# Optimization experiments

Measured on AMD Instinct MI355X. Metric: run time of the kernel, lower is better.

Reference implementation:

```python
import jax, jax.numpy as jnp
import numpy as np

B, L, D, NH = 32, 512, 1024, 1024
T, C = 8, 15          # tables, columns per table
E = T * (1 + C)       # 128 entities (table entity + its column entities)
NCOL = T * C          # 120 column slots == max_entities
K = L // E            # 4 tokens per entity span
TOPK = 6


def setup_inputs() -> dict:
    key = jax.random.key(0)
    ks = jax.random.split(key, 12)
    std = 0.02
    q_enc = jax.random.normal(ks[0], (B, L, D), jnp.float32)
    # contiguous variable-length-style spans: entity e covers tokens [e*K, (e+1)*K)
    entity_tok_idx = jnp.arange(E * K, dtype=jnp.int32).reshape(E, K)
    # entity layout per batch: [tbl0, col0..col14, tbl1, col15..., ...]
    ent = np.arange(E).reshape(T, 1 + C)
    col_entity_idx = jnp.asarray(ent[:, 1:].reshape(-1), jnp.int32)   # [NCOL]
    col_table_idx = jnp.asarray(np.repeat(ent[:, 0], C), jnp.int32)   # [NCOL]
    return {
        "q_enc": q_enc,
        "entity_tok_idx": entity_tok_idx,
        "col_entity_idx": col_entity_idx,
        "col_table_idx": col_table_idx,
        "W_table": jax.random.normal(ks[1], (D, D), jnp.float32) * std,
        "b_table": jnp.zeros((D,), jnp.float32),
        "W_col": jax.random.normal(ks[2], (D, D), jnp.float32) * std,
        "b_col": jnp.zeros((D,), jnp.float32),
        "W_o1": jax.random.normal(ks[3], (D, NH), jnp.float32) * std,
        "b_o1": jnp.zeros((NH,), jnp.float32),
        "W_o2": jax.random.normal(ks[4], (NH, 1), jnp.float32) * std,
        "b_o2": jnp.zeros((1,), jnp.float32),
        "W_t1": jax.random.normal(ks[5], (D, NH), jnp.float32) * std,
        "b_t1": jnp.zeros((NH,), jnp.float32),
        "W_t2": jax.random.normal(ks[6], (NH, TOPK), jnp.float32) * std,
        "b_t2": jnp.zeros((TOPK,), jnp.float32),
    }


def reference(q_enc, entity_tok_idx, col_entity_idx, col_table_idx,
              W_table, b_table, W_col, b_col,
              W_o1, b_o1, W_o2, b_o2,
              W_t1, b_t1, W_t2, b_t2):
    # ragged per-entity token gather + sum pooling (pad+sum in original)
    # q_enc: [B, L, D]; gather -> [B, E, K, D]; segment reduce over K
    encoded_entity = jnp.take(q_enc, entity_tok_idx, axis=1).sum(axis=2)  # [B, E, D]
    # per-column fusion: col_linear(col entity) + table_linear(parent table entity)
    tbl = jnp.einsum("bed,df->bef", encoded_entity[:, col_table_idx], W_table) + b_table
    col = jnp.einsum("bed,df->bef", encoded_entity[:, col_entity_idx], W_col) + b_col
    fused = col + tbl                                                    # [B, NCOL, D]
    att = (jax.nn.relu(fused @ W_o1 + b_o1) @ W_o2 + b_o2)[..., 0]       # [B, NCOL]
    cls = q_enc[:, 0, :]                                                 # [B, D]
    topk = jax.nn.sigmoid(jax.nn.relu(cls @ W_t1 + b_t1) @ W_t2 + b_t2)  # [B, 6]
    return att, topk
```

## Files before the change

kernel.cpp:

```cpp
#include <hip/hip_runtime.h>
#include <hip/hip_bf16.h>

#define BB 32
#define LL 512
#define DD 1024
#define NHD 1024
#define EE 128
#define NCOL 120
#define KTOK 4
#define TOPKN 6
#define MROWS (BB * NCOL)

typedef __attribute__((ext_vector_type(8))) _Float16 f16x8;
typedef __attribute__((ext_vector_type(4))) float f32x4;

__device__ inline ushort f2h(float x) {
    _Float16 h = (_Float16)x;
    union { _Float16 h; ushort u; } c;
    c.h = h;
    return c.u;
}

__global__ __launch_bounds__(256) void ee_kernel(const float* __restrict__ q,
                                                 const int* __restrict__ tok,
                                                 ushort* __restrict__ ee,
                                                 float* __restrict__ att,
                                                 const float* __restrict__ b_o2,
                                                 float* __restrict__ H,
                                                 const float* __restrict__ b_t1) {
    int be = blockIdx.x;
    int b  = be >> 7;
    int e  = be & 127;
    int t  = threadIdx.x;

    if (be < 15) {
        att[be * 256 + t] = b_o2[0];
    } else if (be < 15 + 128) {
        int j = (be - 15) * 256 + t;
        H[j] = b_t1[j & (NHD - 1)];
    }

    const float* qb = q + (size_t)b * LL * DD;
    int t0 = tok[e * KTOK + 0];
    int t1 = tok[e * KTOK + 1];
    int t2 = tok[e * KTOK + 2];
    int t3 = tok[e * KTOK + 3];
    int f = t * 4;
    float4 a = *(const float4*)(qb + (size_t)t0 * DD + f);
    float4 bv = *(const float4*)(qb + (size_t)t1 * DD + f);
    float4 c = *(const float4*)(qb + (size_t)t2 * DD + f);
    float4 d = *(const float4*)(qb + (size_t)t3 * DD + f);
    ushort4 o;
    o.x = f2h(a.x + bv.x + c.x + d.x);
    o.y = f2h(a.y + bv.y + c.y + d.y);
    o.z = f2h(a.z + bv.z + c.z + d.z);
    o.w = f2h(a.w + bv.w + c.w + d.w);
    *(ushort4*)(ee + (size_t)be * DD + f) = o;
}

__global__ __launch_bounds__(256) void pack_w_kernel(
    const float* __restrict__ W0, const float* __restrict__ W1f,
    const float* __restrict__ W2f, ushort* __restrict__ pk0,
    ushort* __restrict__ pk1, ushort* __restrict__ pk2) {
    const float* W = blockIdx.y == 0 ? W0 : (blockIdx.y == 1 ? W1f : W2f);
    ushort* pk     = blockIdx.y == 0 ? pk0 : (blockIdx.y == 1 ? pk1 : pk2);
    int idx = blockIdx.x * 256 + threadIdx.x;
    int l  = idx & 63;
    int kb = (idx >> 6) & 31;
    int nb = idx >> 11;
    int row = kb * 32 + (l >> 4) * 8;
    int col = nb * 16 + (l & 15);
    ushort o[8];
#pragma unroll
    for (int j = 0; j < 8; ++j)
        o[j] = f2h(W[(size_t)(row + j) * NHD + col]);
    ulong2 v;
    v.x = ((ulong)o[0]) | ((ulong)o[1] << 16) | ((ulong)o[2] << 32) | ((ulong)o[3] << 48);
    v.y = ((ulong)o[4]) | ((ulong)o[5] << 16) | ((ulong)o[6] << 32) | ((ulong)o[7] << 48);
    *(ulong2*)(pk + (size_t)idx * 8) = v;
}

__global__ __launch_bounds__(256) void gemm1_kernel(
    const ushort* __restrict__ ee, const int* __restrict__ ci, const int* __restrict__ ti,
    const ushort* __restrict__ Wc_pk, const ushort* __restrict__ Wt_pk,
    const float* __restrict__ bc, const float* __restrict__ bt,
    ushort* __restrict__ fused) {
    int t = threadIdx.x;
    int l = t & 63;
    int w = t >> 6;
    int wm = w >> 1, wn = w & 1;
    int row0 = blockIdx.x * 128 + wm * 64;
    int col0 = blockIdx.y * 64 + wn * 32;
    int nb0  = col0 >> 4;
    int koff = (l >> 4) * 8;

    const ushort* arow0[4];
    const ushort* arow1[4];
#pragma unroll
    for (int m = 0; m < 4; ++m) {
        int r = row0 + m * 16 + (l & 15);
        int b = r / NCOL;
        int i = r - b * NCOL;
        arow0[m] = ee + ((size_t)(b * EE + ci[i])) * DD;
        arow1[m] = ee + ((size_t)(b * EE + ti[i])) * DD;
    }

    f32x4 acc[4][2] = {};

#pragma unroll
    for (int phase = 0; phase < 2; ++phase) {
        const ushort* Wp = phase ? Wt_pk : Wc_pk;
        const ushort* const* ar = phase ? arow1 : arow0;

        f16x8 aA[4], bA[2], aB[4], bB[2];

#define LOAD_FR(AV, BV, kb)                                                     \
        {                                                                       \
            _Pragma("unroll")                                                   \
            for (int m = 0; m < 4; ++m)                                         \
                AV[m] = *(const f16x8*)(ar[m] + (kb) * 32 + koff);              \
            _Pragma("unroll")                                                   \
            for (int n = 0; n < 2; ++n)                                         \
                BV[n] = *(const f16x8*)(Wp + (((size_t)(nb0 + n) * 32 + (kb)) * 64 + l) * 8); \
        }
#define MFMA_FR(AV, BV)                                                         \
        {                                                                       \
            _Pragma("unroll")                                                   \
            for (int m = 0; m < 4; ++m)                                         \
                _Pragma("unroll")                                               \
                for (int n = 0; n < 2; ++n)                                     \
                    acc[m][n] = __builtin_amdgcn_mfma_f32_16x16x32_f16(         \
                        AV[m], BV[n], acc[m][n], 0, 0, 0);                      \
        }

        LOAD_FR(aA, bA, 0)
#pragma unroll 1
        for (int kb = 0; kb < 30; kb += 2) {
            LOAD_FR(aB, bB, kb + 1)
            MFMA_FR(aA, bA)
            LOAD_FR(aA, bA, kb + 2)
            MFMA_FR(aB, bB)
        }
        LOAD_FR(aB, bB, 31)
        MFMA_FR(aA, bA)
        MFMA_FR(aB, bB)
#undef LOAD_FR
#undef MFMA_FR
    }

    float badd[2];
#pragma unroll
    for (int n = 0; n < 2; ++n) {
        int c = col0 + n * 16 + (l & 15);
        badd[n] = bc[c] + bt[c];
    }
    int rlane = (l >> 4) * 4;
#pragma unroll
    for (int m = 0; m < 4; ++m)
#pragma unroll
        for (int n = 0; n < 2; ++n) {
            int c = col0 + n * 16 + (l & 15);
#pragma unroll
            for (int j = 0; j < 4; ++j) {
                int r = row0 + m * 16 + rlane + j;
                fused[(size_t)r * NHD + c] = f2h(acc[m][n][j] + badd[n]);
            }
        }
}

__global__ __launch_bounds__(256) void gemm2_kernel(
    const ushort* __restrict__ fused, const ushort* __restrict__ W1_pk,
    const float* __restrict__ b1, const float* __restrict__ W2,
    float* __restrict__ att) {
    int t = threadIdx.x;
    int l = t & 63;
    int w = t >> 6;
    int wm = w >> 1, wn = w & 1;
    int row0 = blockIdx.x * 128 + wm * 64;
    int col0 = blockIdx.y * 64 + wn * 32;
    int nb0  = col0 >> 4;
    int koff = (l >> 4) * 8;

    const ushort* arow[4];
#pragma unroll
    for (int m = 0; m < 4; ++m)
        arow[m] = fused + (size_t)(row0 + m * 16 + (l & 15)) * NHD;

    f32x4 acc[4][2] = {};
    f16x8 aA[4], bA[2], aB[4], bB[2];

#define LOAD_FR(AV, BV, kb)                                                     \
    {                                                                           \
        _Pragma("unroll")                                                       \
        for (int m = 0; m < 4; ++m)                                             \
            AV[m] = *(const f16x8*)(arow[m] + (kb) * 32 + koff);                \
        _Pragma("unroll")                                                       \
        for (int n = 0; n < 2; ++n)                                             \
            BV[n] = *(const f16x8*)(W1_pk + (((size_t)(nb0 + n) * 32 + (kb)) * 64 + l) * 8); \
    }
#define MFMA_FR(AV, BV)                                                         \
    {                                                                           \
        _Pragma("unroll")                                                       \
        for (int m = 0; m < 4; ++m)                                             \
            _Pragma("unroll")                                                   \
            for (int n = 0; n < 2; ++n)                                         \
                acc[m][n] = __builtin_amdgcn_mfma_f32_16x16x32_f16(             \
                    AV[m], BV[n], acc[m][n], 0, 0, 0);                          \
    }

    LOAD_FR(aA, bA, 0)
#pragma unroll 1
    for (int kb = 0; kb < 30; kb += 2) {
        LOAD_FR(aB, bB, kb + 1)
        MFMA_FR(aA, bA)
        LOAD_FR(aA, bA, kb + 2)
        MFMA_FR(aB, bB)
    }
    LOAD_FR(aB, bB, 31)
    MFMA_FR(aA, bA)
    MFMA_FR(aB, bB)
#undef LOAD_FR
#undef MFMA_FR

    float bo[2], wo[2];
#pragma unroll
    for (int n = 0; n < 2; ++n) {
        int c = col0 + n * 16 + (l & 15);
        bo[n] = b1[c];
        wo[n] = W2[c];
    }
    int rlane = (l >> 4) * 4;
#pragma unroll
    for (int m = 0; m < 4; ++m) {
#pragma unroll
        for (int j = 0; j < 4; ++j) {
            float p = 0.f;
#pragma unroll
            for (int n = 0; n < 2; ++n) {
                float h = fmaxf(acc[m][n][j] + bo[n], 0.f);
                p = fmaf(h, wo[n], p);
            }
            p += __shfl_xor(p, 1);
            p += __shfl_xor(p, 2);
            p += __shfl_xor(p, 4);
            p += __shfl_xor(p, 8);
            if ((l & 15) == 0)
                atomicAdd(&att[row0 + m * 16 + rlane + j], p);
        }
    }
}

__global__ __launch_bounds__(256) void topk_h_kernel(const float* __restrict__ q,
                                                     const float* __restrict__ W1,
                                                     float* __restrict__ H) {
    __shared__ float cls[BB][128];
    __shared__ float wsh[128][17];
    int f0 = blockIdx.x * 16;
    int k0 = blockIdx.y * 128;
    int t = threadIdx.x;
#pragma unroll
    for (int m = 0; m < 16; ++m) {
        int idx = t + m * 256;
        int b = idx >> 7, d = idx & 127;
        cls[b][d] = q[(size_t)b * LL * DD + k0 + d];
    }
#pragma unroll
    for (int m = 0; m < 8; ++m) {
        int idx = t + m * 256;
        int r = idx >> 4, c = idx & 15;
        wsh[r][c] = W1[(size_t)(k0 + r) * NHD + f0 + c];
    }
    __syncthreads();
    int f = t & 15;
    int b0 = t >> 4;
#pragma unroll
    for (int h = 0; h < 2; ++h) {
        int b = b0 + h * 16;
        float s = 0.f;
#pragma unroll 8
        for (int d = 0; d < 128; ++d)
            s = fmaf(cls[b][d], wsh[d][f], s);
        atomicAdd(&H[(size_t)b * NHD + f0 + f], s);
    }
}

__global__ __launch_bounds__(256) void topk_out_kernel(
    const float* __restrict__ H, const float* __restrict__ W2,
    const float* __restrict__ b2, float* __restrict__ outp) {
    __shared__ float red[4][TOPKN];
    int b = blockIdx.x;
    int t = threadIdx.x;
    float part[TOPKN] = {};
#pragma unroll
    for (int m = 0; m < 4; ++m) {
        int f = t + m * 256;
        float h = fmaxf(H[(size_t)b * NHD + f], 0.f);
#pragma unroll
        for (int k = 0; k < TOPKN; ++k)
            part[k] = fmaf(h, W2[f * TOPKN + k], part[k]);
    }
#pragma unroll
    for (int k = 0; k < TOPKN; ++k) {
        float v = part[k];
        for (int off = 1; off < 64; off <<= 1) v += __shfl_xor(v, off);
        part[k] = v;
    }
    int wave = t >> 6, lane = t & 63;
    if (lane == 0)
#pragma unroll
        for (int k = 0; k < TOPKN; ++k) red[wave][k] = part[k];
    __syncthreads();
    if (t == 0)
#pragma unroll
        for (int k = 0; k < TOPKN; ++k) {
            float s = red[0][k] + red[1][k] + red[2][k] + red[3][k] + b2[k];
            outp[b * TOPKN + k] = 1.f / (1.f + __expf(-s));
        }
}

extern "C" void kernel_launch(void* const* d_in, const int* in_sizes, int n_in,
                              void* d_out, int out_size, void* d_ws, size_t ws_size,
                              hipStream_t stream) {
    const float* q_enc   = (const float*)d_in[0];
    const int*   etok    = (const int*)  d_in[1];
    const int*   ci      = (const int*)  d_in[2];
    const int*   ti      = (const int*)  d_in[3];
    const float* W_table = (const float*)d_in[4];
    const float* b_table = (const float*)d_in[5];
    const float* W_col   = (const float*)d_in[6];
    const float* b_col   = (const float*)d_in[7];
    const float* W_o1    = (const float*)d_in[8];
    const float* b_o1    = (const float*)d_in[9];
    const float* W_o2    = (const float*)d_in[10];
    const float* b_o2    = (const float*)d_in[11];
    const float* W_t1    = (const float*)d_in[12];
    const float* b_t1    = (const float*)d_in[13];
    const float* W_t2    = (const float*)d_in[14];
    const float* b_t2    = (const float*)d_in[15];

    float* outp = (float*)d_out;
    float* att  = outp;
    float* topk = outp + MROWS;

    char* ws = (char*)d_ws;
    ushort* ee_h    = (ushort*)(ws);
    ushort* fused   = (ushort*)(ws + 8388608);
    ushort* Wc_pk   = (ushort*)(ws + 16252928);
    ushort* Wt_pk   = (ushort*)(ws + 18350080);
    ushort* Wo1_pk  = (ushort*)(ws + 20447232);
    float*  H       = (float*) (ws + 22544384);

    hipLaunchKernelGGL(ee_kernel, dim3(BB * EE), dim3(256), 0, stream,
                       q_enc, etok, ee_h, att, b_o2, H, b_t1);
    hipLaunchKernelGGL(pack_w_kernel, dim3(512, 3), dim3(256), 0, stream,
                       W_col, W_table, W_o1, Wc_pk, Wt_pk, Wo1_pk);
    hipLaunchKernelGGL(gemm1_kernel, dim3(MROWS / 128, NHD / 64), dim3(256), 0, stream,
                       ee_h, ci, ti, Wc_pk, Wt_pk, b_col, b_table, fused);
    hipLaunchKernelGGL(gemm2_kernel, dim3(MROWS / 128, NHD / 64), dim3(256), 0, stream,
                       fused, Wo1_pk, b_o1, W_o2, att);
    hipLaunchKernelGGL(topk_h_kernel, dim3(64, 8), dim3(256), 0, stream, q_enc, W_t1, H);
    hipLaunchKernelGGL(topk_out_kernel, dim3(BB), dim3(256), 0, stream, H, W_t2, b_t2, topk);
}
```

Baseline: 225.5 us.

## Halve GEMM row tile and deepen register prefetch to three stages

Both GEMM kernels now give each wave a 32x32 output tile instead of 64x32, which doubles the grid to 60x16 blocks. The register pipeline changes from double-buffered to triple-buffered fragment loads, with explicit scalar accumulators. The aim is more blocks and waves across the CUs, plus deeper latency hiding for the direct global loads. In exchange, each B fragment is reused half as often, so global/L2 traffic for weights roughly doubles.

```diff
diff --git a/kernel.cpp b/kernel.cpp
--- a/kernel.cpp
+++ b/kernel.cpp
@@ -80,6 +80,43 @@
     *(ulong2*)(pk + (size_t)idx * 8) = v;
 }
 
+#define DEF_MFMA(A0, A1, B0, B1)                                                \
+    {                                                                           \
+        acc00 = __builtin_amdgcn_mfma_f32_16x16x32_f16(A0, B0, acc00, 0, 0, 0); \
+        acc01 = __builtin_amdgcn_mfma_f32_16x16x32_f16(A0, B1, acc01, 0, 0, 0); \
+        acc10 = __builtin_amdgcn_mfma_f32_16x16x32_f16(A1, B0, acc10, 0, 0, 0); \
+        acc11 = __builtin_amdgcn_mfma_f32_16x16x32_f16(A1, B1, acc11, 0, 0, 0); \
+    }
+
+#define GEMM_PIPE(ar0, ar1, W)                                                  \
+    {                                                                           \
+        const ushort* a0p = (ar0);                                              \
+        const ushort* a1p = (ar1);                                              \
+        const ushort* wp  = (W);                                                \
+        _LD(Aa0, Aa1, Ba0, Ba1, 0)                                              \
+        _LD(Ab0, Ab1, Bb0, Bb1, 1)                                              \
+        _LD(Ac0, Ac1, Bc0, Bc1, 2)                                              \
+        _Pragma("unroll 1")                                                     \
+        for (int kb = 0; kb < 27; kb += 3) {                                    \
+            DEF_MFMA(Aa0, Aa1, Ba0, Ba1) _LD(Aa0, Aa1, Ba0, Ba1, kb + 3)        \
+            DEF_MFMA(Ab0, Ab1, Bb0, Bb1) _LD(Ab0, Ab1, Bb0, Bb1, kb + 4)        \
+            DEF_MFMA(Ac0, Ac1, Bc0, Bc1) _LD(Ac0, Ac1, Bc0, Bc1, kb + 5)        \
+        }                                                                       \
+        DEF_MFMA(Aa0, Aa1, Ba0, Ba1) _LD(Aa0, Aa1, Ba0, Ba1, 30)                \
+        DEF_MFMA(Ab0, Ab1, Bb0, Bb1) _LD(Ab0, Ab1, Bb0, Bb1, 31)                \
+        DEF_MFMA(Ac0, Ac1, Bc0, Bc1)                                            \
+        DEF_MFMA(Aa0, Aa1, Ba0, Ba1)                                            \
+        DEF_MFMA(Ab0, Ab1, Bb0, Bb1)                                            \
+    }
+
+#define _LD(A0, A1, B0, B1, kb)                                                 \
+    {                                                                           \
+        A0 = *(const f16x8*)(a0p + (kb) * 32 + koff);                           \
+        A1 = *(const f16x8*)(a1p + (kb) * 32 + koff);                           \
+        B0 = *(const f16x8*)(wp + (((size_t)nb0 * 32 + (kb)) * 64 + l) * 8);    \
+        B1 = *(const f16x8*)(wp + (((size_t)(nb0 + 1) * 32 + (kb)) * 64 + l) * 8); \
+    }
+
 __global__ __launch_bounds__(256) void gemm1_kernel(
     const ushort* __restrict__ ee, const int* __restrict__ ci, const int* __restrict__ ti,
     const ushort* __restrict__ Wc_pk, const ushort* __restrict__ Wt_pk,
@@ -89,15 +126,15 @@
     int l = t & 63;
     int w = t >> 6;
     int wm = w >> 1, wn = w & 1;
-    int row0 = blockIdx.x * 128 + wm * 64;
+    int row0 = blockIdx.x * 64 + wm * 32;
     int col0 = blockIdx.y * 64 + wn * 32;
     int nb0  = col0 >> 4;
     int koff = (l >> 4) * 8;
 
-    const ushort* arow0[4];
-    const ushort* arow1[4];
-#pragma unroll
-    for (int m = 0; m < 4; ++m) {
+    const ushort* arow0[2];
+    const ushort* arow1[2];
+#pragma unroll
+    for (int m = 0; m < 2; ++m) {
         int r = row0 + m * 16 + (l & 15);
         int b = r / NCOL;
         int i = r - b * NCOL;
@@ -105,48 +142,11 @@
         arow1[m] = ee + ((size_t)(b * EE + ti[i])) * DD;
     }
 
-    f32x4 acc[4][2] = {};
-
-#pragma unroll
-    for (int phase = 0; phase < 2; ++phase) {
-        const ushort* Wp = phase ? Wt_pk : Wc_pk;
-        const ushort* const* ar = phase ? arow1 : arow0;
-
-        f16x8 aA[4], bA[2], aB[4], bB[2];
-
-#define LOAD_FR(AV, BV, kb)                                                     \
-        {                                                                       \
-            _Pragma("unroll")                                                   \
-            for (int m = 0; m < 4; ++m)                                         \
-                AV[m] = *(const f16x8*)(ar[m] + (kb) * 32 + koff);              \
-            _Pragma("unroll")                                                   \
-            for (int n = 0; n < 2; ++n)                                         \
-                BV[n] = *(const f16x8*)(Wp + (((size_t)(nb0 + n) * 32 + (kb)) * 64 + l) * 8); \
-        }
-#define MFMA_FR(AV, BV)                                                         \
-        {                                                                       \
-            _Pragma("unroll")                                                   \
-            for (int m = 0; m < 4; ++m)                                         \
-                _Pragma("unroll")                                               \
-                for (int n = 0; n < 2; ++n)                                     \
-                    acc[m][n] = __builtin_amdgcn_mfma_f32_16x16x32_f16(         \
-                        AV[m], BV[n], acc[m][n], 0, 0, 0);                      \
-        }
-
-        LOAD_FR(aA, bA, 0)
-#pragma unroll 1
-        for (int kb = 0; kb < 30; kb += 2) {
-            LOAD_FR(aB, bB, kb + 1)
-            MFMA_FR(aA, bA)
-            LOAD_FR(aA, bA, kb + 2)
-            MFMA_FR(aB, bB)
-        }
-        LOAD_FR(aB, bB, 31)
-        MFMA_FR(aA, bA)
-        MFMA_FR(aB, bB)
-#undef LOAD_FR
-#undef MFMA_FR
-    }
+    f32x4 acc00 = {}, acc01 = {}, acc10 = {}, acc11 = {};
+    f16x8 Aa0, Aa1, Ba0, Ba1, Ab0, Ab1, Bb0, Bb1, Ac0, Ac1, Bc0, Bc1;
+
+    GEMM_PIPE(arow0[0], arow0[1], Wc_pk)
+    GEMM_PIPE(arow1[0], arow1[1], Wt_pk)
 
     float badd[2];
 #pragma unroll
@@ -155,15 +155,16 @@
         badd[n] = bc[c] + bt[c];
     }
     int rlane = (l >> 4) * 4;
-#pragma unroll
-    for (int m = 0; m < 4; ++m)
+    f32x4 accm[2][2] = {{acc00, acc01}, {acc10, acc11}};
+#pragma unroll
+    for (int m = 0; m < 2; ++m)
 #pragma unroll
         for (int n = 0; n < 2; ++n) {
             int c = col0 + n * 16 + (l & 15);
 #pragma unroll
             for (int j = 0; j < 4; ++j) {
                 int r = row0 + m * 16 + rlane + j;
-                fused[(size_t)r * NHD + c] = f2h(acc[m][n][j] + badd[n]);
+                fused[(size_t)r * NHD + c] = f2h(accm[m][n][j] + badd[n]);
             }
         }
 }
@@ -176,51 +177,20 @@
     int l = t & 63;
     int w = t >> 6;
     int wm = w >> 1, wn = w & 1;
-    int row0 = blockIdx.x * 128 + wm * 64;
+    int row0 = blockIdx.x * 64 + wm * 32;
     int col0 = blockIdx.y * 64 + wn * 32;
     int nb0  = col0 >> 4;
     int koff = (l >> 4) * 8;
 
-    const ushort* arow[4];
-#pragma unroll
-    for (int m = 0; m < 4; ++m)
+    const ushort* arow[2];
+#pragma unroll
+    for (int m = 0; m < 2; ++m)
         arow[m] = fused + (size_t)(row0 + m * 16 + (l & 15)) * NHD;
 
-    f32x4 acc[4][2] = {};
-    f16x8 aA[4], bA[2], aB[4], bB[2];
-
-#define LOAD_FR(AV, BV, kb)                                                     \
-    {                                                                           \
-        _Pragma("unroll")                                                       \
-        for (int m = 0; m < 4; ++m)                                             \
-            AV[m] = *(const f16x8*)(arow[m] + (kb) * 32 + koff);                \
-        _Pragma("unroll")                                                       \
-        for (int n = 0; n < 2; ++n)                                             \
-            BV[n] = *(const f16x8*)(W1_pk + (((size_t)(nb0 + n) * 32 + (kb)) * 64 + l) * 8); \
-    }
-#define MFMA_FR(AV, BV)                                                         \
-    {                                                                           \
-        _Pragma("unroll")                                                       \
-        for (int m = 0; m < 4; ++m)                                             \
-            _Pragma("unroll")                                                   \
-            for (int n = 0; n < 2; ++n)                                         \
-                acc[m][n] = __builtin_amdgcn_mfma_f32_16x16x32_f16(             \
-                    AV[m], BV[n], acc[m][n], 0, 0, 0);                          \
-    }
-
-    LOAD_FR(aA, bA, 0)
-#pragma unroll 1
-    for (int kb = 0; kb < 30; kb += 2) {
-        LOAD_FR(aB, bB, kb + 1)
-        MFMA_FR(aA, bA)
-        LOAD_FR(aA, bA, kb + 2)
-        MFMA_FR(aB, bB)
-    }
-    LOAD_FR(aB, bB, 31)
-    MFMA_FR(aA, bA)
-    MFMA_FR(aB, bB)
-#undef LOAD_FR
-#undef MFMA_FR
+    f32x4 acc00 = {}, acc01 = {}, acc10 = {}, acc11 = {};
+    f16x8 Aa0, Aa1, Ba0, Ba1, Ab0, Ab1, Bb0, Bb1, Ac0, Ac1, Bc0, Bc1;
+
+    GEMM_PIPE(arow[0], arow[1], W1_pk)
 
     float bo[2], wo[2];
 #pragma unroll
@@ -230,14 +200,15 @@
         wo[n] = W2[c];
     }
     int rlane = (l >> 4) * 4;
-#pragma unroll
-    for (int m = 0; m < 4; ++m) {
+    f32x4 accm[2][2] = {{acc00, acc01}, {acc10, acc11}};
+#pragma unroll
+    for (int m = 0; m < 2; ++m) {
 #pragma unroll
         for (int j = 0; j < 4; ++j) {
             float p = 0.f;
 #pragma unroll
             for (int n = 0; n < 2; ++n) {
-                float h = fmaxf(acc[m][n][j] + bo[n], 0.f);
+                float h = fmaxf(accm[m][n][j] + bo[n], 0.f);
                 p = fmaf(h, wo[n], p);
             }
             p += __shfl_xor(p, 1);
@@ -354,9 +325,9 @@
                        q_enc, etok, ee_h, att, b_o2, H, b_t1);
     hipLaunchKernelGGL(pack_w_kernel, dim3(512, 3), dim3(256), 0, stream,
                        W_col, W_table, W_o1, Wc_pk, Wt_pk, Wo1_pk);
-    hipLaunchKernelGGL(gemm1_kernel, dim3(MROWS / 128, NHD / 64), dim3(256), 0, stream,
+    hipLaunchKernelGGL(gemm1_kernel, dim3(MROWS / 64, NHD / 64), dim3(256), 0, stream,
                        ee_h, ci, ti, Wc_pk, Wt_pk, b_col, b_table, fused);
-    hipLaunchKernelGGL(gemm2_kernel, dim3(MROWS / 128, NHD / 64), dim3(256), 0, stream,
+    hipLaunchKernelGGL(gemm2_kernel, dim3(MROWS / 64, NHD / 64), dim3(256), 0, stream,
                        fused, Wo1_pk, b_o1, W_o2, att);
     hipLaunchKernelGGL(topk_h_kernel, dim3(64, 8), dim3(256), 0, stream, q_enc, W_t1, H);
     hipLaunchKernelGGL(topk_out_kernel, dim3(BB), dim3(256), 0, stream, H, W_t2, b_t2, topk);
```

Result: slower. 233.2 us (+3.4%).
